# Kernel tuning notes

Hardware: AMD Instinct MI355X
Metric: run time of the kernel (lower is better)

Reference implementation:

```python
import jax, jax.numpy as jnp
import numpy as np

B, N, D_MODEL, HEADS, DFF, M = 4, 4096, 1024, 16, 4096, 256
DH = D_MODEL // HEADS  # 64
EPS_K = 1e-4
LN_EPS = 1e-5


def setup_inputs() -> dict:
    key = jax.random.key(0)
    ks = jax.random.split(key, 12)
    s = 0.02
    return {
        "video": jax.random.normal(ks[0], (B, N, D_MODEL), jnp.float32),
        "Wq": jax.random.normal(ks[1], (D_MODEL, D_MODEL), jnp.float32) * s,
        "bq": jnp.zeros((D_MODEL,), jnp.float32),
        "Wk": jax.random.normal(ks[2], (D_MODEL, D_MODEL), jnp.float32) * s,
        "bk": jnp.zeros((D_MODEL,), jnp.float32),
        "Wv": jax.random.normal(ks[3], (D_MODEL, D_MODEL), jnp.float32) * s,
        "bv": jnp.zeros((D_MODEL,), jnp.float32),
        "Wo": jax.random.normal(ks[4], (D_MODEL, D_MODEL), jnp.float32) * s,
        "bo": jnp.zeros((D_MODEL,), jnp.float32),
        "proj": jax.random.normal(ks[5], (M, DH), jnp.float32),  # random-feature matrix (buffer)
        "W1": jax.random.normal(ks[6], (DFF, D_MODEL), jnp.float32) * s,
        "b1": jnp.zeros((DFF,), jnp.float32),
        "W2": jax.random.normal(ks[7], (D_MODEL, DFF), jnp.float32) * s,
        "b2": jnp.zeros((D_MODEL,), jnp.float32),
        "g2": jnp.ones((D_MODEL,), jnp.float32),
        "be2": jnp.zeros((D_MODEL,), jnp.float32),
        "g3": jnp.ones((D_MODEL,), jnp.float32),
        "be3": jnp.zeros((D_MODEL,), jnp.float32),
    }


def softmax_kernel(x, proj, is_query):
    # FAVOR+ positive softmax random features (Performer).
    # x: [b,h,n,dh], proj: [m,dh]
    norm = x.shape[-1] ** -0.25  # data normalizer 1/d^{1/4}
    ratio = proj.shape[0] ** -0.5
    xp = jnp.einsum("bhnd,md->bhnm", x * norm, proj)
    diag = jnp.sum(jnp.square(x), axis=-1, keepdims=True) * 0.5 * (norm * norm)
    if is_query:
        stab = jnp.max(xp, axis=-1, keepdims=True)
    else:
        stab = jnp.max(xp, axis=(-1, -2), keepdims=True)
    return ratio * (jnp.exp(xp - diag - stab) + EPS_K)


def layer_norm(x, g, b):
    mu = jnp.mean(x, axis=-1, keepdims=True)
    var = jnp.mean(jnp.square(x - mu), axis=-1, keepdims=True)
    return (x - mu) * jax.lax.rsqrt(var + LN_EPS) * g + b


def reference(video, Wq, bq, Wk, bk, Wv, bv, Wo, bo, proj,
              W1, b1, W2, b2, g2, be2, g3, be3):
    b, n, d = video.shape
    split = lambda t: t.reshape(b, n, HEADS, DH).transpose(0, 2, 1, 3)  # [b,h,n,dh]
    q = split(video @ Wq.T + bq)
    k = split(video @ Wk.T + bk)
    v = split(video @ Wv.T + bv)

    qp = softmax_kernel(q, proj, is_query=True)   # [b,h,n,m]
    kp = softmax_kernel(k, proj, is_query=False)  # [b,h,n,m]

    # Non-causal linear attention: O(n*m*dh) instead of O(n^2)
    k_sum = jnp.sum(kp, axis=2)                              # [b,h,m]
    denom = jnp.einsum("bhnm,bhm->bhn", qp, k_sum)           # [b,h,n]
    ctx = jnp.einsum("bhnm,bhnd->bhmd", kp, v)               # [b,h,m,dh]
    out = jnp.einsum("bhnm,bhmd->bhnd", qp, ctx) / denom[..., None]

    attn = out.transpose(0, 2, 1, 3).reshape(b, n, d) @ Wo.T + bo
    x = layer_norm(video + attn, g2, be2)  # dropout is identity in eval
    ff = jax.nn.relu(x @ W1.T + b1) @ W2.T + b2
    return layer_norm(x + ff, g3, be3)
```

## Files before the change

### kernel.cpp

```cpp
#include <hip/hip_runtime.h>
#include <hip/hip_bf16.h>

#define N_TOK   4096
#define DMODEL  1024
#define NHEADS  16
#define DH      64
#define MFEAT   256
#define DFF     4096
#define BATCH   4
#define ROWS    (BATCH * N_TOK)

#define NORMF      0.35355339059327373f
#define HALF_NORM2 0.0625f
#define RATIO      0.0625f
#define EPSK       1e-4f
#define LNEPS      1e-5f

typedef unsigned short ushort_t;
using bfrag = __attribute__((ext_vector_type(8))) short;
using facc  = __attribute__((ext_vector_type(4))) float;
using ush8  = __attribute__((ext_vector_type(8))) unsigned short;

__device__ __forceinline__ float b2f(ushort_t u) {
    return __bfloat162float(__builtin_bit_cast(__hip_bfloat16, u));
}
__device__ __forceinline__ ushort_t f2b(float f) {
    return __builtin_bit_cast(ushort_t, __float2bfloat16(f));
}
__device__ __forceinline__ void stC(float* p, float v) { *p = v; }
__device__ __forceinline__ void stC(ushort_t* p, float v) { *p = f2b(v); }

__device__ __forceinline__ void gload_lds16(const void* g, void* l) {
    __builtin_amdgcn_global_load_lds(
        (const __attribute__((address_space(1))) unsigned int*)g,
        (__attribute__((address_space(3))) unsigned int*)l, 16, 0, 0);
}

__device__ __forceinline__ unsigned fkey(float f) {
    unsigned u = __float_as_uint(f);
    return (u & 0x80000000u) ? ~u : (u | 0x80000000u);
}
__device__ __forceinline__ float fdec(unsigned k) {
    return (k & 0x80000000u) ? __uint_as_float(k ^ 0x80000000u) : __uint_as_float(~k);
}

__global__ __launch_bounds__(256) void cvt_bf16(const float* __restrict__ s,
                                                ushort_t* __restrict__ d, int n4) {
    int i = blockIdx.x * 256 + threadIdx.x;
    if (i >= n4) return;
    float4 v = ((const float4*)s)[i];
    ((ushort4*)d)[i] = make_ushort4(f2b(v.x), f2b(v.y), f2b(v.z), f2b(v.w));
}

template <int FJ, typename OT>
__global__ __launch_bounds__(256) void gemm_mfma(
    const ushort_t* __restrict__ A, const ushort_t* __restrict__ W,
    const float* __restrict__ bias, OT* __restrict__ C,
    int Nout, int K, int relu)
{
    constexpr int BN = FJ * 32;
    __shared__ short As[128 * 32];
    __shared__ short Ws[BN * 32];
    const int t = threadIdx.x;
    const unsigned nwg = gridDim.x * gridDim.y;
    const unsigned flat = blockIdx.y * gridDim.x + blockIdx.x;
    const unsigned cpx = nwg >> 3;
    const unsigned wg = (flat & 7) * cpx + (flat >> 3);
    const int m0 = (int)(wg / gridDim.x) * 128, n0 = (int)(wg % gridDim.x) * BN;
    const int lane = t & 63, wave = t >> 6;
    const int wr = (wave >> 1) * 64, wc = (wave & 1) * (FJ * 16);
    const int lm = lane & 15, kq = (lane >> 4) * 8;
    facc acc[4][FJ];
#pragma unroll
    for (int i = 0; i < 4; ++i)
#pragma unroll
        for (int j = 0; j < FJ; ++j) acc[i][j] = (facc){0.f, 0.f, 0.f, 0.f};

    for (int k0 = 0; k0 < K; k0 += 32) {
#pragma unroll
        for (int it = 0; it < 2; ++it) {
            int ch = t + it * 256;
            int row = ch >> 2, c8 = (ch & 3) * 8;
            gload_lds16(A + (size_t)(m0 + row) * K + k0 + c8, &As[ch * 8]);
        }
#pragma unroll
        for (int it = 0; it < BN / 64; ++it) {
            int ch = t + it * 256;
            int row = ch >> 2, c8 = (ch & 3) * 8;
            gload_lds16(W + (size_t)(n0 + row) * K + k0 + c8, &Ws[ch * 8]);
        }
        __syncthreads();
        bfrag af[4], bf[FJ];
#pragma unroll
        for (int i = 0; i < 4; ++i) af[i] = *(bfrag*)&As[(wr + i * 16 + lm) * 32 + kq];
#pragma unroll
        for (int j = 0; j < FJ; ++j) bf[j] = *(bfrag*)&Ws[(wc + j * 16 + lm) * 32 + kq];
#pragma unroll
        for (int i = 0; i < 4; ++i)
#pragma unroll
            for (int j = 0; j < FJ; ++j)
                acc[i][j] = __builtin_amdgcn_mfma_f32_16x16x32_bf16(af[i], bf[j], acc[i][j], 0, 0, 0);
        __syncthreads();
    }
    const int rq = (lane >> 4) * 4;
#pragma unroll
    for (int i = 0; i < 4; ++i)
#pragma unroll
        for (int j = 0; j < FJ; ++j) {
            int col = n0 + wc + j * 16 + lm;
            float bc = bias[col];
#pragma unroll
            for (int r = 0; r < 4; ++r) {
                int row = m0 + wr + i * 16 + rq + r;
                float v = acc[i][j][r] + bc;
                if (relu) v = fmaxf(v, 0.f);
                stC(C + (size_t)row * Nout + col, v);
            }
        }
}

__global__ __launch_bounds__(256) void vt_kernel(
    const ushort_t* __restrict__ V, ushort_t* __restrict__ VT)
{
    __shared__ ushort_t tile[64][68];
    const int t = threadIdx.x;
    const int n0 = blockIdx.x * 64, h = blockIdx.y;
#pragma unroll
    for (int i = 0; i < 4; ++i) {
        int idx = t + i * 256;
        int nl = idx >> 4, d4 = (idx & 15) * 4;
        ushort4 v = *(const ushort4*)(V + (size_t)(n0 + nl) * DMODEL + h * DH + d4);
        tile[nl][d4 + 0] = v.x; tile[nl][d4 + 1] = v.y;
        tile[nl][d4 + 2] = v.z; tile[nl][d4 + 3] = v.w;
    }
    __syncthreads();
#pragma unroll
    for (int i = 0; i < 4; ++i) {
        int idx = t + i * 256;
        int d = idx >> 4, n4 = (idx & 15) * 4;
        ushort4 o = make_ushort4(tile[n4][d], tile[n4 + 1][d], tile[n4 + 2][d], tile[n4 + 3][d]);
        *(ushort4*)(VT + (size_t)h * DH * N_TOK + (size_t)d * N_TOK + n0 + n4) = o;
    }
}

__global__ __launch_bounds__(256) void diagk_kernel(
    const ushort_t* __restrict__ Kb, float* __restrict__ diagK)
{
    const int lane = threadIdx.x & 63, wave = threadIdx.x >> 6;
    const int n = blockIdx.x * 4 + wave;
    const ushort_t* kr = Kb + (size_t)n * DMODEL + lane * 16;
    ush8 a = *(const ush8*)kr;
    ush8 b = *(const ush8*)(kr + 8);
    float s = 0.f;
#pragma unroll
    for (int e = 0; e < 8; ++e) { float x = b2f(a[e]); s += x * x; }
#pragma unroll
    for (int e = 0; e < 8; ++e) { float x = b2f(b[e]); s += x * x; }
    s += __shfl_xor(s, 1);
    s += __shfl_xor(s, 2);
    if ((lane & 3) == 0) diagK[(size_t)(lane >> 2) * N_TOK + n] = s;
}

__global__ __launch_bounds__(256) void xk_kernel(
    const ushort_t* __restrict__ projBF,
    const ushort_t* __restrict__ Kb,
    const float* __restrict__ diagK,
    unsigned* __restrict__ kmax16,
    ushort_t* __restrict__ KP,
    int mode)
{
    __shared__ short As[128 * 32];
    __shared__ short Ws[128 * 32];
    const int t = threadIdx.x;
    const int m0 = blockIdx.x * 128, n0 = blockIdx.y * 128, h = blockIdx.z;
    const ushort_t* Kh = Kb + h * DH;
    const int lane = t & 63, wave = t >> 6;
    const int wr = (wave >> 1) * 64, wc = (wave & 1) * 64;
    const int lm = lane & 15, kq = (lane >> 4) * 8;
    facc acc[4][4];
#pragma unroll
    for (int i = 0; i < 4; ++i)
#pragma unroll
        for (int j = 0; j < 4; ++j) acc[i][j] = (facc){0.f, 0.f, 0.f, 0.f};

    for (int k0 = 0; k0 < DH; k0 += 32) {
#pragma unroll
        for (int it = 0; it < 2; ++it) {
            int ch = t + it * 256;
            int row = ch >> 2, c8 = (ch & 3) * 8;
            gload_lds16(projBF + (size_t)(m0 + row) * DH + k0 + c8, &As[ch * 8]);
            gload_lds16(Kh + (size_t)(n0 + row) * DMODEL + k0 + c8, &Ws[ch * 8]);
        }
        __syncthreads();
        bfrag af[4], bf[4];
#pragma unroll
        for (int i = 0; i < 4; ++i) af[i] = *(bfrag*)&As[(wr + i * 16 + lm) * 32 + kq];
#pragma unroll
        for (int j = 0; j < 4; ++j) bf[j] = *(bfrag*)&Ws[(wc + j * 16 + lm) * 32 + kq];
#pragma unroll
        for (int i = 0; i < 4; ++i)
#pragma unroll
            for (int j = 0; j < 4; ++j)
                acc[i][j] = __builtin_amdgcn_mfma_f32_16x16x32_bf16(af[i], bf[j], acc[i][j], 0, 0, 0);
        __syncthreads();
    }
    const int rq = (lane >> 4) * 4;
    if (mode == 0) {
        float mx = -1e30f;
#pragma unroll
        for (int i = 0; i < 4; ++i)
#pragma unroll
            for (int j = 0; j < 4; ++j)
#pragma unroll
                for (int r = 0; r < 4; ++r) mx = fmaxf(mx, acc[i][j][r]);
        mx *= NORMF;
#pragma unroll
        for (int o = 32; o >= 1; o >>= 1) mx = fmaxf(mx, __shfl_xor(mx, o));
        if (lane == 0) atomicMax(kmax16 + h, fkey(mx));
    } else {
        const float stab = fdec(kmax16[h]);
        ushort_t* kb = KP + (size_t)h * MFEAT * N_TOK;
#pragma unroll
        for (int j = 0; j < 4; ++j) {
            int n = n0 + wc + j * 16 + lm;
            float dg = HALF_NORM2 * diagK[(size_t)h * N_TOK + n] + stab;
#pragma unroll
            for (int i = 0; i < 4; ++i)
#pragma unroll
                for (int r = 0; r < 4; ++r) {
                    int m = m0 + wr + i * 16 + rq + r;
                    float x = NORMF * acc[i][j][r];
                    kb[(size_t)m * N_TOK + n] = f2b(RATIO * (expf(x - dg) + EPSK));
                }
        }
    }
}

__global__ __launch_bounds__(256) void ksum_kernel(
    const ushort_t* __restrict__ KP, float* __restrict__ ksum)
{
    const int lane = threadIdx.x & 63, wave = threadIdx.x >> 6;
    const int row = blockIdx.x * 4 + wave;
    const ushort_t* kr = KP + (size_t)row * N_TOK;
    float s = 0.f;
#pragma unroll
    for (int it = 0; it < 8; ++it) {
        ush8 v = *(const ush8*)(kr + it * 512 + lane * 8);
#pragma unroll
        for (int e = 0; e < 8; ++e) s += b2f(v[e]);
    }
#pragma unroll
    for (int o = 32; o >= 1; o >>= 1) s += __shfl_xor(s, o);
    if (lane == 0) ksum[row] = s;
}

__global__ __launch_bounds__(256) void ctx_mfma(
    const ushort_t* __restrict__ KP, const ushort_t* __restrict__ VT,
    float* __restrict__ ctx)
{
    __shared__ short As[128 * 32];
    __shared__ short Vs[64 * 32];
    const int t = threadIdx.x;
    const int z = blockIdx.x, mh = blockIdx.y, h = blockIdx.z;
    const ushort_t* A = KP + (size_t)h * MFEAT * N_TOK + (size_t)mh * 128 * N_TOK;
    const ushort_t* W = VT + (size_t)h * DH * N_TOK;
    const int lane = t & 63, wave = t >> 6;
    const int wr = (wave >> 1) * 64, wc = (wave & 1) * 32;
    const int lm = lane & 15, kq = (lane >> 4) * 8;
    facc acc[4][2];
#pragma unroll
    for (int i = 0; i < 4; ++i)
#pragma unroll
        for (int j = 0; j < 2; ++j) acc[i][j] = (facc){0.f, 0.f, 0.f, 0.f};

    const int kbeg = z * 512, kend = kbeg + 512;
    for (int k0 = kbeg; k0 < kend; k0 += 32) {
#pragma unroll
        for (int it = 0; it < 2; ++it) {
            int ch = t + it * 256;
            int row = ch >> 2, c8 = (ch & 3) * 8;
            gload_lds16(A + (size_t)row * N_TOK + k0 + c8, &As[ch * 8]);
        }
        {
            int row = t >> 2, c8 = (t & 3) * 8;
            gload_lds16(W + (size_t)row * N_TOK + k0 + c8, &Vs[t * 8]);
        }
        __syncthreads();
        bfrag af[4], bf[2];
#pragma unroll
        for (int i = 0; i < 4; ++i) af[i] = *(bfrag*)&As[(wr + i * 16 + lm) * 32 + kq];
#pragma unroll
        for (int j = 0; j < 2; ++j) bf[j] = *(bfrag*)&Vs[(wc + j * 16 + lm) * 32 + kq];
#pragma unroll
        for (int i = 0; i < 4; ++i)
#pragma unroll
            for (int j = 0; j < 2; ++j)
                acc[i][j] = __builtin_amdgcn_mfma_f32_16x16x32_bf16(af[i], bf[j], acc[i][j], 0, 0, 0);
        __syncthreads();
    }
    const int rq = (lane >> 4) * 4;
    float* cb = ctx + (size_t)h * MFEAT * DH + (size_t)mh * 128 * DH;
#pragma unroll
    for (int i = 0; i < 4; ++i)
#pragma unroll
        for (int j = 0; j < 2; ++j)
#pragma unroll
            for (int r = 0; r < 4; ++r) {
                int m = wr + i * 16 + rq + r;
                int d = wc + j * 16 + lm;
                atomicAdd(cb + (size_t)m * DH + d, acc[i][j][r]);
            }
}

__global__ __launch_bounds__(256) void ctx_transpose(
    const float* __restrict__ ctx, ushort_t* __restrict__ ctxT)
{
    __shared__ float tile[64][65];
    const int bh = blockIdx.x, t = threadIdx.x;
    const float* cb = ctx + (size_t)bh * MFEAT * DH;
    ushort_t* ob = ctxT + (size_t)bh * DH * MFEAT;
    for (int mb = 0; mb < 4; ++mb) {
#pragma unroll
        for (int i = 0; i < 16; ++i) {
            int idx = t + i * 256;
            tile[idx >> 6][idx & 63] = cb[(size_t)(mb * 64 + (idx >> 6)) * DH + (idx & 63)];
        }
        __syncthreads();
#pragma unroll
        for (int i = 0; i < 16; ++i) {
            int idx = t + i * 256;
            ob[(size_t)(idx >> 6) * MFEAT + mb * 64 + (idx & 63)] = f2b(tile[idx & 63][idx >> 6]);
        }
        __syncthreads();
    }
}

__global__ __launch_bounds__(256) void xp_gemm(
    const float* __restrict__ Q, const ushort_t* __restrict__ projBF,
    ushort_t* __restrict__ XP)
{
    __shared__ short As[128][40];
    __shared__ short Ws[128][40];
    const int t = threadIdx.x;
    const int m0 = blockIdx.x * 128, n0v = blockIdx.y * 128, h = blockIdx.z;
    const float* Qb = Q + h * DH;
    const int lane = t & 63, wave = t >> 6;
    const int wr = (wave >> 1) * 64, wc = (wave & 1) * 64;
    const int lm = lane & 15, kq = (lane >> 4) * 8;
    facc acc[4][4];
#pragma unroll
    for (int i = 0; i < 4; ++i)
#pragma unroll
        for (int j = 0; j < 4; ++j) acc[i][j] = (facc){0.f, 0.f, 0.f, 0.f};

    for (int k0 = 0; k0 < 64; k0 += 32) {
#pragma unroll
        for (int it = 0; it < 4; ++it) {
            int ch = t + it * 256;
            int row = ch >> 3, c4 = (ch & 7) * 4;
            float4 v = *(const float4*)(Qb + (size_t)(n0v + row) * DMODEL + k0 + c4);
            As[row][c4 + 0] = (short)f2b(v.x);
            As[row][c4 + 1] = (short)f2b(v.y);
            As[row][c4 + 2] = (short)f2b(v.z);
            As[row][c4 + 3] = (short)f2b(v.w);
        }
#pragma unroll
        for (int it = 0; it < 2; ++it) {
            int ch = t + it * 256;
            int row = ch >> 2, c8 = (ch & 3) * 8;
            *(uint4*)&Ws[row][c8] = *(const uint4*)(projBF + (size_t)(m0 + row) * DH + k0 + c8);
        }
        __syncthreads();
        bfrag af[4], bf[4];
#pragma unroll
        for (int i = 0; i < 4; ++i) af[i] = *(bfrag*)&As[wr + i * 16 + lm][kq];
#pragma unroll
        for (int j = 0; j < 4; ++j) bf[j] = *(bfrag*)&Ws[wc + j * 16 + lm][kq];
#pragma unroll
        for (int i = 0; i < 4; ++i)
#pragma unroll
            for (int j = 0; j < 4; ++j)
                acc[i][j] = __builtin_amdgcn_mfma_f32_16x16x32_bf16(af[i], bf[j], acc[i][j], 0, 0, 0);
        __syncthreads();
    }
    const int rq = (lane >> 4) * 4;
    ushort_t* xb = XP + (size_t)h * N_TOK * MFEAT;
#pragma unroll
    for (int i = 0; i < 4; ++i)
#pragma unroll
        for (int j = 0; j < 4; ++j) {
            int col = m0 + wc + j * 16 + lm;
#pragma unroll
            for (int r = 0; r < 4; ++r) {
                int row = n0v + wr + i * 16 + rq + r;
                xb[(size_t)row * MFEAT + col] = f2b(NORMF * acc[i][j][r]);
            }
        }
}

__global__ __launch_bounds__(256) void qp_kernel(
    ushort_t* __restrict__ XP, const float* __restrict__ Q,
    const float* __restrict__ ksum, float* __restrict__ denom)
{
    const int lane = threadIdx.x & 63, wave = threadIdx.x >> 6;
    const int row0 = (blockIdx.x * 4 + wave) * 8;
    for (int rr = 0; rr < 8; ++rr) {
        const int row = row0 + rr;
        const int h = row >> 12, n = row & 4095;
        ushort_t* xr = XP + (size_t)row * MFEAT + lane * 4;
        ushort4 xv = *(ushort4*)xr;
        float x0 = b2f(xv.x), x1 = b2f(xv.y), x2 = b2f(xv.z), x3 = b2f(xv.w);
        float qv = Q[(size_t)n * DMODEL + h * DH + lane];
        float ss = qv * qv;
#pragma unroll
        for (int o = 32; o >= 1; o >>= 1) ss += __shfl_xor(ss, o);
        float mx = fmaxf(fmaxf(x0, x1), fmaxf(x2, x3));
#pragma unroll
        for (int o = 32; o >= 1; o >>= 1) mx = fmaxf(mx, __shfl_xor(mx, o));
        const float sh = HALF_NORM2 * ss + mx;
        float p0 = RATIO * (expf(x0 - sh) + EPSK);
        float p1 = RATIO * (expf(x1 - sh) + EPSK);
        float p2 = RATIO * (expf(x2 - sh) + EPSK);
        float p3 = RATIO * (expf(x3 - sh) + EPSK);
        ushort4 pv = make_ushort4(f2b(p0), f2b(p1), f2b(p2), f2b(p3));
        *(ushort4*)xr = pv;
        float4 ks4 = *(const float4*)(ksum + h * MFEAT + lane * 4);
        float dn = b2f(pv.x) * ks4.x + b2f(pv.y) * ks4.y + b2f(pv.z) * ks4.z + b2f(pv.w) * ks4.w;
#pragma unroll
        for (int o = 32; o >= 1; o >>= 1) dn += __shfl_xor(dn, o);
        if (lane == 0) denom[row] = dn;
    }
}

__global__ __launch_bounds__(256) void out_gemm(
    const ushort_t* __restrict__ XP, const ushort_t* __restrict__ ctxT,
    const float* __restrict__ denom, ushort_t* __restrict__ OUT)
{
    __shared__ short As[128 * 32];
    __shared__ short Ws[64 * 32];
    const int t = threadIdx.x;
    const int n0 = blockIdx.x * 128, h = blockIdx.y;
    const ushort_t* A = XP + (size_t)h * N_TOK * MFEAT;
    const ushort_t* W = ctxT + (size_t)h * DH * MFEAT;
    const float* dnb = denom + (size_t)h * N_TOK;
    ushort_t* ob = OUT + h * DH;
    const int lane = t & 63, wave = t >> 6;
    const int wr = (wave >> 1) * 64, wc = (wave & 1) * 32;
    const int lm = lane & 15, kq = (lane >> 4) * 8;
    facc acc[4][2];
#pragma unroll
    for (int i = 0; i < 4; ++i)
#pragma unroll
        for (int j = 0; j < 2; ++j) acc[i][j] = (facc){0.f, 0.f, 0.f, 0.f};

    for (int k0 = 0; k0 < MFEAT; k0 += 32) {
#pragma unroll
        for (int it = 0; it < 2; ++it) {
            int ch = t + it * 256;
            int row = ch >> 2, c8 = (ch & 3) * 8;
            gload_lds16(A + (size_t)(n0 + row) * MFEAT + k0 + c8, &As[ch * 8]);
        }
        {
            int row = t >> 2, c8 = (t & 3) * 8;
            gload_lds16(W + (size_t)row * MFEAT + k0 + c8, &Ws[t * 8]);
        }
        __syncthreads();
        bfrag af[4], bf[2];
#pragma unroll
        for (int i = 0; i < 4; ++i) af[i] = *(bfrag*)&As[(wr + i * 16 + lm) * 32 + kq];
#pragma unroll
        for (int j = 0; j < 2; ++j) bf[j] = *(bfrag*)&Ws[(wc + j * 16 + lm) * 32 + kq];
#pragma unroll
        for (int i = 0; i < 4; ++i)
#pragma unroll
            for (int j = 0; j < 2; ++j)
                acc[i][j] = __builtin_amdgcn_mfma_f32_16x16x32_bf16(af[i], bf[j], acc[i][j], 0, 0, 0);
        __syncthreads();
    }
    const int rq = (lane >> 4) * 4;
#pragma unroll
    for (int i = 0; i < 4; ++i)
#pragma unroll
        for (int r = 0; r < 4; ++r) {
            int row = n0 + wr + i * 16 + rq + r;
            float inv = 1.f / dnb[row];
#pragma unroll
            for (int j = 0; j < 2; ++j) {
                int col = wc + j * 16 + lm;
                ob[(size_t)row * DMODEL + col] = f2b(acc[i][j][r] * inv);
            }
        }
}

__global__ __launch_bounds__(256) void ln_kernel(
    const float* __restrict__ A, const void* __restrict__ Badd, int badd_bf16,
    const float* __restrict__ g, const float* __restrict__ bb,
    float* __restrict__ out, ushort_t* __restrict__ out_bf)
{
    __shared__ float red[256];
    const int row = blockIdx.x, t = threadIdx.x;
    const float* a = A + (size_t)row * DMODEL;
    float v[4];
    float s = 0.f;
#pragma unroll
    for (int i = 0; i < 4; ++i) {
        int col = t + i * 256;
        float add = badd_bf16 ? b2f(((const ushort_t*)Badd)[(size_t)row * DMODEL + col])
                              : ((const float*)Badd)[(size_t)row * DMODEL + col];
        v[i] = a[col] + add;
        s += v[i];
    }
    red[t] = s;
    __syncthreads();
    for (int st = 128; st > 0; st >>= 1) { if (t < st) red[t] += red[t + st]; __syncthreads(); }
    float mu = red[0] * (1.f / DMODEL);
    __syncthreads();
    float sq = 0.f;
#pragma unroll
    for (int i = 0; i < 4; ++i) { float dlt = v[i] - mu; sq += dlt * dlt; }
    red[t] = sq;
    __syncthreads();
    for (int st = 128; st > 0; st >>= 1) { if (t < st) red[t] += red[t + st]; __syncthreads(); }
    float rstd = rsqrtf(red[0] * (1.f / DMODEL) + LNEPS);
    float* o = out + (size_t)row * DMODEL;
#pragma unroll
    for (int i = 0; i < 4; ++i) {
        int col = t + i * 256;
        float val = (v[i] - mu) * rstd * g[col] + bb[col];
        o[col] = val;
        if (out_bf) out_bf[(size_t)row * DMODEL + col] = f2b(val);
    }
}

extern "C" void kernel_launch(void* const* d_in, const int* in_sizes, int n_in,
                              void* d_out, int out_size, void* d_ws, size_t ws_size,
                              hipStream_t stream)
{
    const float* video = (const float*)d_in[0];
    const float* Wq = (const float*)d_in[1];
    const float* bq = (const float*)d_in[2];
    const float* Wk = (const float*)d_in[3];
    const float* bk = (const float*)d_in[4];
    const float* Wv = (const float*)d_in[5];
    const float* bv = (const float*)d_in[6];
    const float* Wo = (const float*)d_in[7];
    const float* bo = (const float*)d_in[8];
    const float* proj = (const float*)d_in[9];
    const float* W1 = (const float*)d_in[10];
    const float* b1 = (const float*)d_in[11];
    const float* W2 = (const float*)d_in[12];
    const float* b2 = (const float*)d_in[13];
    const float* g2 = (const float*)d_in[14];
    const float* be2 = (const float*)d_in[15];
    const float* g3 = (const float*)d_in[16];
    const float* be3 = (const float*)d_in[17];

    char* ws = (char*)d_ws;
    const size_t MB = 1048576ull;
    ushort_t* videoBF = (ushort_t*)(ws + 0);
    ushort_t* Kb   = (ushort_t*)(ws + 32 * MB);
    ushort_t* XBFb = (ushort_t*)(ws + 32 * MB);
    ushort_t* Vb   = (ushort_t*)(ws + 40 * MB);
    ushort_t* Fb   = (ushort_t*)(ws + 40 * MB);
    ushort_t* VTb  = (ushort_t*)(ws + 48 * MB);
    ushort_t* Yb   = (ushort_t*)(ws + 48 * MB);
    ushort_t* KP   = (ushort_t*)(ws + 56 * MB);
    ushort_t* Hb   = (ushort_t*)(ws + 56 * MB);
    float*    ctxb = (float*)(ws + 93847552ull);
    ushort_t* ctxTb = (ushort_t*)(ws + 93847552ull + MB);
    char* smalls = ws + 91 * MB + 393216ull;
    float*    diagK  = (float*)(smalls);
    float*    ksum   = (float*)(smalls + 262144);
    float*    denomB = (float*)(smalls + 278528);
    unsigned* kmax16 = (unsigned*)(smalls + 540672);
    ushort_t* projBF = (ushort_t*)(smalls + 541184);
    ushort_t* OUTb = (ushort_t*)(ws + 92 * MB);
    ushort_t* WqBF = (ushort_t*)(ws + 100 * MB);
    ushort_t* WkBF = (ushort_t*)(ws + 102 * MB);
    ushort_t* WvBF = (ushort_t*)(ws + 104 * MB);
    ushort_t* WoBF = (ushort_t*)(ws + 106 * MB);
    ushort_t* W1BF = (ushort_t*)(ws + 108 * MB);
    ushort_t* W2BF = (ushort_t*)(ws + 116 * MB);
    float* Qbuf = (float*)d_out;

    dim3 blk(256);

    cvt_bf16<<<dim3(ROWS * DMODEL / 1024), blk, 0, stream>>>(video, videoBF, ROWS * DMODEL / 4);
    cvt_bf16<<<dim3(DMODEL * DMODEL / 1024), blk, 0, stream>>>(Wq, WqBF, DMODEL * DMODEL / 4);
    cvt_bf16<<<dim3(DMODEL * DMODEL / 1024), blk, 0, stream>>>(Wk, WkBF, DMODEL * DMODEL / 4);
    cvt_bf16<<<dim3(DMODEL * DMODEL / 1024), blk, 0, stream>>>(Wv, WvBF, DMODEL * DMODEL / 4);
    cvt_bf16<<<dim3(DMODEL * DMODEL / 1024), blk, 0, stream>>>(Wo, WoBF, DMODEL * DMODEL / 4);
    cvt_bf16<<<dim3(DFF * DMODEL / 1024), blk, 0, stream>>>(W1, W1BF, DFF * DMODEL / 4);
    cvt_bf16<<<dim3(DFF * DMODEL / 1024), blk, 0, stream>>>(W2, W2BF, DFF * DMODEL / 4);
    cvt_bf16<<<dim3(16), blk, 0, stream>>>(proj, projBF, MFEAT * DH / 4);

    gemm_mfma<4, float><<<dim3(8, ROWS / 128), blk, 0, stream>>>(
        videoBF, WqBF, bq, Qbuf, DMODEL, DMODEL, 0);

    dim3 gP(8, 32);

    for (int b = 0; b < BATCH; ++b) {
        const size_t roff = (size_t)b * N_TOK;
        const ushort_t* vbf = videoBF + roff * DMODEL;
        float* Qb = Qbuf + roff * DMODEL;

        gemm_mfma<4, ushort_t><<<gP, blk, 0, stream>>>(vbf, WkBF, bk, Kb, DMODEL, DMODEL, 0);
        gemm_mfma<4, ushort_t><<<gP, blk, 0, stream>>>(vbf, WvBF, bv, Vb, DMODEL, DMODEL, 0);
        vt_kernel<<<dim3(64, 16), blk, 0, stream>>>(Vb, VTb);
        diagk_kernel<<<dim3(1024), blk, 0, stream>>>(Kb, diagK);

        hipMemsetAsync(ctxb, 0, MB, stream);
        hipMemsetAsync(kmax16, 0, 64, stream);

        xk_kernel<<<dim3(2, 32, 16), blk, 0, stream>>>(projBF, Kb, diagK, kmax16, KP, 0);
        xk_kernel<<<dim3(2, 32, 16), blk, 0, stream>>>(projBF, Kb, diagK, kmax16, KP, 1);
        ksum_kernel<<<dim3(1024), blk, 0, stream>>>(KP, ksum);
        ctx_mfma<<<dim3(8, 2, 16), blk, 0, stream>>>(KP, VTb, ctxb);
        ctx_transpose<<<dim3(16), blk, 0, stream>>>(ctxb, ctxTb);

        xp_gemm<<<dim3(2, 32, 16), blk, 0, stream>>>(Qb, projBF, KP);
        qp_kernel<<<dim3(2048), blk, 0, stream>>>(KP, Qb, ksum, denomB);
        out_gemm<<<dim3(32, 16), blk, 0, stream>>>(KP, ctxTb, denomB, OUTb);

        gemm_mfma<4, ushort_t><<<gP, blk, 0, stream>>>(OUTb, WoBF, bo, Yb, DMODEL, DMODEL, 0);
        ln_kernel<<<dim3(N_TOK), blk, 0, stream>>>(
            video + roff * DMODEL, Yb, 1, g2, be2, Qb, XBFb);
        gemm_mfma<4, ushort_t><<<dim3(32, 32), blk, 0, stream>>>(
            XBFb, W1BF, b1, Hb, DFF, DMODEL, 1);
        gemm_mfma<2, ushort_t><<<dim3(16, 32), blk, 0, stream>>>(
            Hb, W2BF, b2, Fb, DMODEL, DFF, 0);
        ln_kernel<<<dim3(N_TOK), blk, 0, stream>>>(
            Qb, Fb, 1, g3, be3, Qb, nullptr);
    }
}
```

Before: 1.760 ms.

## Double-buffer GEMM LDS tiles, fuse K/V projections, deterministic ctx reduction, shuffle LayerNorm

All MFMA GEMM kernels now use two LDS buffers so the next K-slice's global-to-LDS copy is issued before the current slice's MFMAs, aiming to hide load latency behind compute. The K and V projections are merged into one launch over a doubled grid. The ctx split-K step stores per-split partials that the transpose kernel sums, which removes the atomics and the memset. The transpose grid also grows from 16 to 64 blocks. LayerNorm switches to float4 loads and wave-shuffle reductions. Doubling LDS per block may lower occupancy, and ctxp reuses the OUTb region, which is only safe because of stream ordering.

After: 1.658 ms. -5.8%, faster.

```diff
diff --git a/kernel.cpp b/kernel.cpp
--- a/kernel.cpp
+++ b/kernel.cpp
@@ -59,8 +59,8 @@
     int Nout, int K, int relu)
 {
     constexpr int BN = FJ * 32;
-    __shared__ short As[128 * 32];
-    __shared__ short Ws[BN * 32];
+    __shared__ short As[2][128 * 32];
+    __shared__ short Ws[2][BN * 32];
     const int t = threadIdx.x;
     const unsigned nwg = gridDim.x * gridDim.y;
     const unsigned flat = blockIdx.y * gridDim.x + blockIdx.x;
@@ -76,31 +76,36 @@
 #pragma unroll
         for (int j = 0; j < FJ; ++j) acc[i][j] = (facc){0.f, 0.f, 0.f, 0.f};
 
-    for (int k0 = 0; k0 < K; k0 += 32) {
+    auto stage = [&](int b, int k0) {
 #pragma unroll
         for (int it = 0; it < 2; ++it) {
             int ch = t + it * 256;
-            int row = ch >> 2, c8 = (ch & 3) * 8;
-            gload_lds16(A + (size_t)(m0 + row) * K + k0 + c8, &As[ch * 8]);
+            gload_lds16(A + (size_t)(m0 + (ch >> 2)) * K + k0 + (ch & 3) * 8, &As[b][ch * 8]);
         }
 #pragma unroll
         for (int it = 0; it < BN / 64; ++it) {
             int ch = t + it * 256;
-            int row = ch >> 2, c8 = (ch & 3) * 8;
-            gload_lds16(W + (size_t)(n0 + row) * K + k0 + c8, &Ws[ch * 8]);
-        }
-        __syncthreads();
+            gload_lds16(W + (size_t)(n0 + (ch >> 2)) * K + k0 + (ch & 3) * 8, &Ws[b][ch * 8]);
+        }
+    };
+
+    stage(0, 0);
+    __syncthreads();
+    int buf = 0;
+    for (int k0 = 0; k0 < K; k0 += 32) {
+        if (k0 + 32 < K) stage(buf ^ 1, k0 + 32);
         bfrag af[4], bf[FJ];
 #pragma unroll
-        for (int i = 0; i < 4; ++i) af[i] = *(bfrag*)&As[(wr + i * 16 + lm) * 32 + kq];
-#pragma unroll
-        for (int j = 0; j < FJ; ++j) bf[j] = *(bfrag*)&Ws[(wc + j * 16 + lm) * 32 + kq];
+        for (int i = 0; i < 4; ++i) af[i] = *(bfrag*)&As[buf][(wr + i * 16 + lm) * 32 + kq];
+#pragma unroll
+        for (int j = 0; j < FJ; ++j) bf[j] = *(bfrag*)&Ws[buf][(wc + j * 16 + lm) * 32 + kq];
 #pragma unroll
         for (int i = 0; i < 4; ++i)
 #pragma unroll
             for (int j = 0; j < FJ; ++j)
                 acc[i][j] = __builtin_amdgcn_mfma_f32_16x16x32_bf16(af[i], bf[j], acc[i][j], 0, 0, 0);
         __syncthreads();
+        buf ^= 1;
     }
     const int rq = (lane >> 4) * 4;
 #pragma unroll
@@ -115,6 +120,76 @@
                 float v = acc[i][j][r] + bc;
                 if (relu) v = fmaxf(v, 0.f);
                 stC(C + (size_t)row * Nout + col, v);
+            }
+        }
+}
+
+__global__ __launch_bounds__(256) void gemm_kv(
+    const ushort_t* __restrict__ A,
+    const ushort_t* __restrict__ WK, const ushort_t* __restrict__ WV,
+    const float* __restrict__ bK, const float* __restrict__ bV,
+    ushort_t* __restrict__ CK, ushort_t* __restrict__ CV)
+{
+    __shared__ short As[2][128 * 32];
+    __shared__ short Ws[2][128 * 32];
+    const int t = threadIdx.x;
+    const unsigned nwg = gridDim.x * gridDim.y;
+    const unsigned flat = blockIdx.y * gridDim.x + blockIdx.x;
+    const unsigned cpx = nwg >> 3;
+    const unsigned wg = (flat & 7) * cpx + (flat >> 3);
+    const int m0 = (int)(wg / gridDim.x) * 128;
+    const int nt = (int)(wg % gridDim.x);
+    const ushort_t* W = (nt < 8) ? WK : WV;
+    const float* bias = (nt < 8) ? bK : bV;
+    ushort_t* C = (nt < 8) ? CK : CV;
+    const int n0 = (nt & 7) * 128;
+    const int lane = t & 63, wave = t >> 6;
+    const int wr = (wave >> 1) * 64, wc = (wave & 1) * 64;
+    const int lm = lane & 15, kq = (lane >> 4) * 8;
+    facc acc[4][4];
+#pragma unroll
+    for (int i = 0; i < 4; ++i)
+#pragma unroll
+        for (int j = 0; j < 4; ++j) acc[i][j] = (facc){0.f, 0.f, 0.f, 0.f};
+
+    auto stage = [&](int b, int k0) {
+#pragma unroll
+        for (int it = 0; it < 2; ++it) {
+            int ch = t + it * 256;
+            gload_lds16(A + (size_t)(m0 + (ch >> 2)) * DMODEL + k0 + (ch & 3) * 8, &As[b][ch * 8]);
+            gload_lds16(W + (size_t)(n0 + (ch >> 2)) * DMODEL + k0 + (ch & 3) * 8, &Ws[b][ch * 8]);
+        }
+    };
+
+    stage(0, 0);
+    __syncthreads();
+    int buf = 0;
+    for (int k0 = 0; k0 < DMODEL; k0 += 32) {
+        if (k0 + 32 < DMODEL) stage(buf ^ 1, k0 + 32);
+        bfrag af[4], bf[4];
+#pragma unroll
+        for (int i = 0; i < 4; ++i) af[i] = *(bfrag*)&As[buf][(wr + i * 16 + lm) * 32 + kq];
+#pragma unroll
+        for (int j = 0; j < 4; ++j) bf[j] = *(bfrag*)&Ws[buf][(wc + j * 16 + lm) * 32 + kq];
+#pragma unroll
+        for (int i = 0; i < 4; ++i)
+#pragma unroll
+            for (int j = 0; j < 4; ++j)
+                acc[i][j] = __builtin_amdgcn_mfma_f32_16x16x32_bf16(af[i], bf[j], acc[i][j], 0, 0, 0);
+        __syncthreads();
+        buf ^= 1;
+    }
+    const int rq = (lane >> 4) * 4;
+#pragma unroll
+    for (int i = 0; i < 4; ++i)
+#pragma unroll
+        for (int j = 0; j < 4; ++j) {
+            int col = n0 + wc + j * 16 + lm;
+            float bc = bias[col];
+#pragma unroll
+            for (int r = 0; r < 4; ++r) {
+                int row = m0 + wr + i * 16 + rq + r;
+                C[(size_t)row * DMODEL + col] = f2b(acc[i][j][r] + bc);
             }
         }
 }
@@ -169,8 +244,8 @@
     ushort_t* __restrict__ KP,
     int mode)
 {
-    __shared__ short As[128 * 32];
-    __shared__ short Ws[128 * 32];
+    __shared__ short As[2][128 * 32];
+    __shared__ short Ws[2][128 * 32];
     const int t = threadIdx.x;
     const int m0 = blockIdx.x * 128, n0 = blockIdx.y * 128, h = blockIdx.z;
     const ushort_t* Kh = Kb + h * DH;
@@ -183,26 +258,32 @@
 #pragma unroll
         for (int j = 0; j < 4; ++j) acc[i][j] = (facc){0.f, 0.f, 0.f, 0.f};
 
-    for (int k0 = 0; k0 < DH; k0 += 32) {
+    auto stage = [&](int b, int k0) {
 #pragma unroll
         for (int it = 0; it < 2; ++it) {
             int ch = t + it * 256;
-            int row = ch >> 2, c8 = (ch & 3) * 8;
-            gload_lds16(projBF + (size_t)(m0 + row) * DH + k0 + c8, &As[ch * 8]);
-            gload_lds16(Kh + (size_t)(n0 + row) * DMODEL + k0 + c8, &Ws[ch * 8]);
-        }
-        __syncthreads();
+            gload_lds16(projBF + (size_t)(m0 + (ch >> 2)) * DH + k0 + (ch & 3) * 8, &As[b][ch * 8]);
+            gload_lds16(Kh + (size_t)(n0 + (ch >> 2)) * DMODEL + k0 + (ch & 3) * 8, &Ws[b][ch * 8]);
+        }
+    };
+
+    stage(0, 0);
+    __syncthreads();
+    int buf = 0;
+    for (int k0 = 0; k0 < DH; k0 += 32) {
+        if (k0 + 32 < DH) stage(buf ^ 1, k0 + 32);
         bfrag af[4], bf[4];
 #pragma unroll
-        for (int i = 0; i < 4; ++i) af[i] = *(bfrag*)&As[(wr + i * 16 + lm) * 32 + kq];
-#pragma unroll
-        for (int j = 0; j < 4; ++j) bf[j] = *(bfrag*)&Ws[(wc + j * 16 + lm) * 32 + kq];
+        for (int i = 0; i < 4; ++i) af[i] = *(bfrag*)&As[buf][(wr + i * 16 + lm) * 32 + kq];
+#pragma unroll
+        for (int j = 0; j < 4; ++j) bf[j] = *(bfrag*)&Ws[buf][(wc + j * 16 + lm) * 32 + kq];
 #pragma unroll
         for (int i = 0; i < 4; ++i)
 #pragma unroll
             for (int j = 0; j < 4; ++j)
                 acc[i][j] = __builtin_amdgcn_mfma_f32_16x16x32_bf16(af[i], bf[j], acc[i][j], 0, 0, 0);
         __syncthreads();
+        buf ^= 1;
     }
     const int rq = (lane >> 4) * 4;
     if (mode == 0) {
@@ -256,10 +337,10 @@
 
 __global__ __launch_bounds__(256) void ctx_mfma(
     const ushort_t* __restrict__ KP, const ushort_t* __restrict__ VT,
-    float* __restrict__ ctx)
-{
-    __shared__ short As[128 * 32];
-    __shared__ short Vs[64 * 32];
+    float* __restrict__ ctxp)
+{
+    __shared__ short As[2][128 * 32];
+    __shared__ short Vs[2][64 * 32];
     const int t = threadIdx.x;
     const int z = blockIdx.x, mh = blockIdx.y, h = blockIdx.z;
     const ushort_t* A = KP + (size_t)h * MFEAT * N_TOK + (size_t)mh * 128 * N_TOK;
@@ -273,33 +354,36 @@
 #pragma unroll
         for (int j = 0; j < 2; ++j) acc[i][j] = (facc){0.f, 0.f, 0.f, 0.f};
 
-    const int kbeg = z * 512, kend = kbeg + 512;
-    for (int k0 = kbeg; k0 < kend; k0 += 32) {
+    auto stage = [&](int b, int k0) {
 #pragma unroll
         for (int it = 0; it < 2; ++it) {
             int ch = t + it * 256;
-            int row = ch >> 2, c8 = (ch & 3) * 8;
-            gload_lds16(A + (size_t)row * N_TOK + k0 + c8, &As[ch * 8]);
-        }
-        {
-            int row = t >> 2, c8 = (t & 3) * 8;
-            gload_lds16(W + (size_t)row * N_TOK + k0 + c8, &Vs[t * 8]);
-        }
-        __syncthreads();
+            gload_lds16(A + (size_t)(ch >> 2) * N_TOK + k0 + (ch & 3) * 8, &As[b][ch * 8]);
+        }
+        gload_lds16(W + (size_t)(t >> 2) * N_TOK + k0 + (t & 3) * 8, &Vs[b][t * 8]);
+    };
+
+    const int kbeg = z * 512, kend = kbeg + 512;
+    stage(0, kbeg);
+    __syncthreads();
+    int buf = 0;
+    for (int k0 = kbeg; k0 < kend; k0 += 32) {
+        if (k0 + 32 < kend) stage(buf ^ 1, k0 + 32);
         bfrag af[4], bf[2];
 #pragma unroll
-        for (int i = 0; i < 4; ++i) af[i] = *(bfrag*)&As[(wr + i * 16 + lm) * 32 + kq];
-#pragma unroll
-        for (int j = 0; j < 2; ++j) bf[j] = *(bfrag*)&Vs[(wc + j * 16 + lm) * 32 + kq];
+        for (int i = 0; i < 4; ++i) af[i] = *(bfrag*)&As[buf][(wr + i * 16 + lm) * 32 + kq];
+#pragma unroll
+        for (int j = 0; j < 2; ++j) bf[j] = *(bfrag*)&Vs[buf][(wc + j * 16 + lm) * 32 + kq];
 #pragma unroll
         for (int i = 0; i < 4; ++i)
 #pragma unroll
             for (int j = 0; j < 2; ++j)
                 acc[i][j] = __builtin_amdgcn_mfma_f32_16x16x32_bf16(af[i], bf[j], acc[i][j], 0, 0, 0);
         __syncthreads();
+        buf ^= 1;
     }
     const int rq = (lane >> 4) * 4;
-    float* cb = ctx + (size_t)h * MFEAT * DH + (size_t)mh * 128 * DH;
+    float* cb = ctxp + ((size_t)(z * NHEADS + h) * MFEAT + mh * 128) * DH;
 #pragma unroll
     for (int i = 0; i < 4; ++i)
 #pragma unroll
@@ -308,30 +392,33 @@
             for (int r = 0; r < 4; ++r) {
                 int m = wr + i * 16 + rq + r;
                 int d = wc + j * 16 + lm;
-                atomicAdd(cb + (size_t)m * DH + d, acc[i][j][r]);
+                cb[(size_t)m * DH + d] = acc[i][j][r];
             }
 }
 
 __global__ __launch_bounds__(256) void ctx_transpose(
-    const float* __restrict__ ctx, ushort_t* __restrict__ ctxT)
+    const float* __restrict__ ctxp, ushort_t* __restrict__ ctxT)
 {
     __shared__ float tile[64][65];
-    const int bh = blockIdx.x, t = threadIdx.x;
-    const float* cb = ctx + (size_t)bh * MFEAT * DH;
-    ushort_t* ob = ctxT + (size_t)bh * DH * MFEAT;
-    for (int mb = 0; mb < 4; ++mb) {
-#pragma unroll
-        for (int i = 0; i < 16; ++i) {
-            int idx = t + i * 256;
-            tile[idx >> 6][idx & 63] = cb[(size_t)(mb * 64 + (idx >> 6)) * DH + (idx & 63)];
-        }
-        __syncthreads();
-#pragma unroll
-        for (int i = 0; i < 16; ++i) {
-            int idx = t + i * 256;
-            ob[(size_t)(idx >> 6) * MFEAT + mb * 64 + (idx & 63)] = f2b(tile[idx & 63][idx >> 6]);
-        }
-        __syncthreads();
+    const int h = blockIdx.x >> 2, mb = blockIdx.x & 3, t = threadIdx.x;
+#pragma unroll
+    for (int i = 0; i < 16; ++i) {
+        int idx = t + i * 256;
+        int ml = idx >> 6, d = idx & 63;
+        int m = mb * 64 + ml;
+        float s = 0.f;
+#pragma unroll
+        for (int z = 0; z < 8; ++z)
+            s += ctxp[((size_t)(z * NHEADS + h) * MFEAT + m) * DH + d];
+        tile[ml][d] = s;
+    }
+    __syncthreads();
+    ushort_t* ob = ctxT + (size_t)h * DH * MFEAT;
+#pragma unroll
+    for (int i = 0; i < 16; ++i) {
+        int idx = t + i * 256;
+        int d = idx >> 6, ml = idx & 63;
+        ob[(size_t)d * MFEAT + mb * 64 + ml] = f2b(tile[ml][d]);
     }
 }
 
@@ -436,8 +523,8 @@
     const ushort_t* __restrict__ XP, const ushort_t* __restrict__ ctxT,
     const float* __restrict__ denom, ushort_t* __restrict__ OUT)
 {
-    __shared__ short As[128 * 32];
-    __shared__ short Ws[64 * 32];
+    __shared__ short As[2][128 * 32];
+    __shared__ short Ws[2][64 * 32];
     const int t = threadIdx.x;
     const int n0 = blockIdx.x * 128, h = blockIdx.y;
     const ushort_t* A = XP + (size_t)h * N_TOK * MFEAT;
@@ -453,29 +540,32 @@
 #pragma unroll
         for (int j = 0; j < 2; ++j) acc[i][j] = (facc){0.f, 0.f, 0.f, 0.f};
 
-    for (int k0 = 0; k0 < MFEAT; k0 += 32) {
+    auto stage = [&](int b, int k0) {
 #pragma unroll
         for (int it = 0; it < 2; ++it) {
             int ch = t + it * 256;
-            int row = ch >> 2, c8 = (ch & 3) * 8;
-            gload_lds16(A + (size_t)(n0 + row) * MFEAT + k0 + c8, &As[ch * 8]);
-        }
-        {
-            int row = t >> 2, c8 = (t & 3) * 8;
-            gload_lds16(W + (size_t)row * MFEAT + k0 + c8, &Ws[t * 8]);
-        }
-        __syncthreads();
+            gload_lds16(A + (size_t)(n0 + (ch >> 2)) * MFEAT + k0 + (ch & 3) * 8, &As[b][ch * 8]);
+        }
+        gload_lds16(W + (size_t)(t >> 2) * MFEAT + k0 + (t & 3) * 8, &Ws[b][t * 8]);
+    };
+
+    stage(0, 0);
+    __syncthreads();
+    int buf = 0;
+    for (int k0 = 0; k0 < MFEAT; k0 += 32) {
+        if (k0 + 32 < MFEAT) stage(buf ^ 1, k0 + 32);
         bfrag af[4], bf[2];
 #pragma unroll
-        for (int i = 0; i < 4; ++i) af[i] = *(bfrag*)&As[(wr + i * 16 + lm) * 32 + kq];
-#pragma unroll
-        for (int j = 0; j < 2; ++j) bf[j] = *(bfrag*)&Ws[(wc + j * 16 + lm) * 32 + kq];
+        for (int i = 0; i < 4; ++i) af[i] = *(bfrag*)&As[buf][(wr + i * 16 + lm) * 32 + kq];
+#pragma unroll
+        for (int j = 0; j < 2; ++j) bf[j] = *(bfrag*)&Ws[buf][(wc + j * 16 + lm) * 32 + kq];
 #pragma unroll
         for (int i = 0; i < 4; ++i)
 #pragma unroll
             for (int j = 0; j < 2; ++j)
                 acc[i][j] = __builtin_amdgcn_mfma_f32_16x16x32_bf16(af[i], bf[j], acc[i][j], 0, 0, 0);
         __syncthreads();
+        buf ^= 1;
     }
     const int rq = (lane >> 4) * 4;
 #pragma unroll
@@ -497,39 +587,42 @@
     const float* __restrict__ g, const float* __restrict__ bb,
     float* __restrict__ out, ushort_t* __restrict__ out_bf)
 {
-    __shared__ float red[256];
+    __shared__ float red[8];
     const int row = blockIdx.x, t = threadIdx.x;
-    const float* a = A + (size_t)row * DMODEL;
-    float v[4];
-    float s = 0.f;
-#pragma unroll
-    for (int i = 0; i < 4; ++i) {
-        int col = t + i * 256;
-        float add = badd_bf16 ? b2f(((const ushort_t*)Badd)[(size_t)row * DMODEL + col])
-                              : ((const float*)Badd)[(size_t)row * DMODEL + col];
-        v[i] = a[col] + add;
-        s += v[i];
-    }
-    red[t] = s;
-    __syncthreads();
-    for (int st = 128; st > 0; st >>= 1) { if (t < st) red[t] += red[t + st]; __syncthreads(); }
-    float mu = red[0] * (1.f / DMODEL);
-    __syncthreads();
-    float sq = 0.f;
-#pragma unroll
-    for (int i = 0; i < 4; ++i) { float dlt = v[i] - mu; sq += dlt * dlt; }
-    red[t] = sq;
-    __syncthreads();
-    for (int st = 128; st > 0; st >>= 1) { if (t < st) red[t] += red[t + st]; __syncthreads(); }
-    float rstd = rsqrtf(red[0] * (1.f / DMODEL) + LNEPS);
-    float* o = out + (size_t)row * DMODEL;
-#pragma unroll
-    for (int i = 0; i < 4; ++i) {
-        int col = t + i * 256;
-        float val = (v[i] - mu) * rstd * g[col] + bb[col];
-        o[col] = val;
-        if (out_bf) out_bf[(size_t)row * DMODEL + col] = f2b(val);
-    }
+    const int lane = t & 63, wave = t >> 6;
+    float4 av = ((const float4*)(A + (size_t)row * DMODEL))[t];
+    float a0, a1, a2, a3;
+    if (badd_bf16) {
+        ushort4 bv4 = ((const ushort4*)Badd)[(size_t)row * (DMODEL / 4) + t];
+        a0 = b2f(bv4.x); a1 = b2f(bv4.y); a2 = b2f(bv4.z); a3 = b2f(bv4.w);
+    } else {
+        float4 bf4 = ((const float4*)Badd)[(size_t)row * (DMODEL / 4) + t];
+        a0 = bf4.x; a1 = bf4.y; a2 = bf4.z; a3 = bf4.w;
+    }
+    float v0 = av.x + a0, v1 = av.y + a1, v2 = av.z + a2, v3 = av.w + a3;
+    float s = v0 + v1 + v2 + v3;
+#pragma unroll
+    for (int o = 32; o >= 1; o >>= 1) s += __shfl_xor(s, o);
+    if (lane == 0) red[wave] = s;
+    __syncthreads();
+    float mu = (red[0] + red[1] + red[2] + red[3]) * (1.f / DMODEL);
+    float d0 = v0 - mu, d1 = v1 - mu, d2 = v2 - mu, d3 = v3 - mu;
+    float sq = d0 * d0 + d1 * d1 + d2 * d2 + d3 * d3;
+#pragma unroll
+    for (int o = 32; o >= 1; o >>= 1) sq += __shfl_xor(sq, o);
+    if (lane == 0) red[4 + wave] = sq;
+    __syncthreads();
+    float rstd = rsqrtf((red[4] + red[5] + red[6] + red[7]) * (1.f / DMODEL) + LNEPS);
+    float4 gv = ((const float4*)g)[t];
+    float4 bv = ((const float4*)bb)[t];
+    float o0 = d0 * rstd * gv.x + bv.x;
+    float o1 = d1 * rstd * gv.y + bv.y;
+    float o2 = d2 * rstd * gv.z + bv.z;
+    float o3 = d3 * rstd * gv.w + bv.w;
+    ((float4*)(out + (size_t)row * DMODEL))[t] = make_float4(o0, o1, o2, o3);
+    if (out_bf)
+        ((ushort4*)(out_bf + (size_t)row * DMODEL))[t] =
+            make_ushort4(f2b(o0), f2b(o1), f2b(o2), f2b(o3));
 }
 
 extern "C" void kernel_launch(void* const* d_in, const int* in_sizes, int n_in,
@@ -566,7 +659,6 @@
     ushort_t* Yb   = (ushort_t*)(ws + 48 * MB);
     ushort_t* KP   = (ushort_t*)(ws + 56 * MB);
     ushort_t* Hb   = (ushort_t*)(ws + 56 * MB);
-    float*    ctxb = (float*)(ws + 93847552ull);
     ushort_t* ctxTb = (ushort_t*)(ws + 93847552ull + MB);
     char* smalls = ws + 91 * MB + 393216ull;
     float*    diagK  = (float*)(smalls);
@@ -574,6 +666,7 @@
     float*    denomB = (float*)(smalls + 278528);
     unsigned* kmax16 = (unsigned*)(smalls + 540672);
     ushort_t* projBF = (ushort_t*)(smalls + 541184);
+    float*    ctxp  = (float*)(ws + 92 * MB);
     ushort_t* OUTb = (ushort_t*)(ws + 92 * MB);
     ushort_t* WqBF = (ushort_t*)(ws + 100 * MB);
     ushort_t* WkBF = (ushort_t*)(ws + 102 * MB);
@@ -604,19 +697,17 @@
         const ushort_t* vbf = videoBF + roff * DMODEL;
         float* Qb = Qbuf + roff * DMODEL;
 
-        gemm_mfma<4, ushort_t><<<gP, blk, 0, stream>>>(vbf, WkBF, bk, Kb, DMODEL, DMODEL, 0);
-        gemm_mfma<4, ushort_t><<<gP, blk, 0, stream>>>(vbf, WvBF, bv, Vb, DMODEL, DMODEL, 0);
+        gemm_kv<<<dim3(16, 32), blk, 0, stream>>>(vbf, WkBF, WvBF, bk, bv, Kb, Vb);
         vt_kernel<<<dim3(64, 16), blk, 0, stream>>>(Vb, VTb);
         diagk_kernel<<<dim3(1024), blk, 0, stream>>>(Kb, diagK);
 
-        hipMemsetAsync(ctxb, 0, MB, stream);
         hipMemsetAsync(kmax16, 0, 64, stream);
 
         xk_kernel<<<dim3(2, 32, 16), blk, 0, stream>>>(projBF, Kb, diagK, kmax16, KP, 0);
         xk_kernel<<<dim3(2, 32, 16), blk, 0, stream>>>(projBF, Kb, diagK, kmax16, KP, 1);
         ksum_kernel<<<dim3(1024), blk, 0, stream>>>(KP, ksum);
-        ctx_mfma<<<dim3(8, 2, 16), blk, 0, stream>>>(KP, VTb, ctxb);
-        ctx_transpose<<<dim3(16), blk, 0, stream>>>(ctxb, ctxTb);
+        ctx_mfma<<<dim3(8, 2, 16), blk, 0, stream>>>(KP, VTb, ctxp);
+        ctx_transpose<<<dim3(64), blk, 0, stream>>>(ctxp, ctxTb);
 
         xp_gemm<<<dim3(2, 32, 16), blk, 0, stream>>>(Qb, projBF, KP);
         qp_kernel<<<dim3(2048), blk, 0, stream>>>(KP, Qb, ksum, denomB);
```
